# Kernel tuning notes

Measured on AMD Instinct MI355X. Metric: run time of the kernel, lower is better.

The kernel has to match this reference:

```python
import jax, jax.numpy as jnp
import numpy as np

B_, L, D_MODEL = 8, 2048, 512
EXPAND, D_STATE, HEADDIM, NGROUPS, D_CONV = 2, 16, 64, 1, 4
D_INNER = EXPAND * D_MODEL            # 1024
NHEADS = D_INNER // HEADDIM           # 16
CONV_DIM = D_INNER + 2 * NGROUPS * D_STATE   # 1056
D_IN_PROJ = 2 * D_INNER + 2 * NGROUPS * D_STATE + NHEADS  # 2096
EPS = 1e-5


def _mamba_params(key):
    ks = jax.random.split(key, 5)
    in_proj_w = jax.random.normal(ks[0], (D_IN_PROJ, D_MODEL), jnp.float32) * (D_MODEL ** -0.5)
    conv_w = jax.random.normal(ks[1], (CONV_DIM, 1, D_CONV), jnp.float32) * (D_CONV ** -0.5)
    conv_b = jnp.zeros((CONV_DIM,), jnp.float32)
    # inverse-softplus of dt ~ U[1e-3, 0.1] (mamba-ssm style init)
    dt_bias = jnp.log(jnp.expm1(jax.random.uniform(ks[2], (NHEADS,), jnp.float32, 1e-3, 0.1)))
    A_log = jnp.log(jax.random.uniform(ks[3], (NHEADS,), jnp.float32, 1.0, 16.0))
    Dp = jnp.ones((NHEADS,), jnp.float32)
    norm_w = jnp.ones((D_INNER,), jnp.float32)
    out_proj_w = jax.random.normal(ks[4], (D_MODEL, D_INNER), jnp.float32) * (D_INNER ** -0.5)
    return [in_proj_w, conv_w, conv_b, dt_bias, A_log, Dp, norm_w, out_proj_w]


def setup_inputs() -> dict:
    key = jax.random.key(0)
    k0, k1, k2 = jax.random.split(key, 3)
    d = {"x": jax.random.normal(k0, (B_, L, D_MODEL), jnp.float32)}
    names = ["in_proj_w", "conv_w", "conv_b", "dt_bias", "A_log", "Dp", "norm_w", "out_proj_w"]
    for pre, k in (("fwd_", k1), ("bwd_", k2)):
        for n, p in zip(names, _mamba_params(k)):
            d[pre + n] = p
    return d


def _silu(v):
    return v * jax.nn.sigmoid(v)


def _mamba2(u, in_proj_w, conv_w, conv_b, dt_bias, A_log, Dp, norm_w, out_proj_w):
    b, l, _ = u.shape
    zxbcdt = u @ in_proj_w.T                                # (b,l,D_IN_PROJ)
    z, xBC, dt = jnp.split(zxbcdt, [D_INNER, D_INNER + CONV_DIM], axis=-1)
    # causal depthwise conv1d + silu
    xc = jnp.transpose(xBC, (0, 2, 1))                      # (b,C,l)
    xc = jax.lax.conv_general_dilated(xc, conv_w, (1,), [(D_CONV - 1, 0)],
                                      feature_group_count=CONV_DIM)
    xBC = _silu(jnp.transpose(xc, (0, 2, 1)) + conv_b)      # (b,l,C)
    xs, Bm, Cm = jnp.split(xBC, [D_INNER, D_INNER + NGROUPS * D_STATE], axis=-1)
    xs = xs.reshape(b, l, NHEADS, HEADDIM)
    Bm = Bm.reshape(b, l, NGROUPS, D_STATE)[:, :, 0]        # ngroups=1 -> (b,l,N)
    Cm = Cm.reshape(b, l, NGROUPS, D_STATE)[:, :, 0]
    dt = jax.nn.softplus(dt + dt_bias)                      # (b,l,H)
    A = -jnp.exp(A_log)                                     # (H,)
    dA = jnp.exp(dt * A)                                    # (b,l,H), in (0,1)

    def step(h, inp):
        dA_t, dt_t, x_t, B_t, C_t = inp
        h = h * dA_t[:, :, None, None] + jnp.einsum('bh,bhp,bn->bhpn', dt_t, x_t, B_t)
        y = jnp.einsum('bhpn,bn->bhp', h, C_t)
        return h, y

    h0 = jnp.zeros((b, NHEADS, HEADDIM, D_STATE), u.dtype)
    seq = (jnp.moveaxis(dA, 1, 0), jnp.moveaxis(dt, 1, 0), jnp.moveaxis(xs, 1, 0),
           jnp.moveaxis(Bm, 1, 0), jnp.moveaxis(Cm, 1, 0))
    _, ys = jax.lax.scan(step, h0, seq)
    y = jnp.moveaxis(ys, 0, 1) + xs * Dp[None, None, :, None]   # (b,l,H,P)
    y = y.reshape(b, l, D_INNER)
    # RMSNormGated (norm_before_gate=False): rmsnorm(y * silu(z)) * w
    y = y * _silu(z)
    y = y * jax.lax.rsqrt(jnp.mean(y * y, axis=-1, keepdims=True) + EPS) * norm_w
    return y @ out_proj_w.T


def reference(x,
              fwd_in_proj_w, fwd_conv_w, fwd_conv_b, fwd_dt_bias, fwd_A_log, fwd_Dp, fwd_norm_w, fwd_out_proj_w,
              bwd_in_proj_w, bwd_conv_w, bwd_conv_b, bwd_dt_bias, bwd_A_log, bwd_Dp, bwd_norm_w, bwd_out_proj_w):
    fwd = _mamba2(x, fwd_in_proj_w, fwd_conv_w, fwd_conv_b, fwd_dt_bias, fwd_A_log, fwd_Dp, fwd_norm_w, fwd_out_proj_w)
    bwd = _mamba2(x[:, ::-1], bwd_in_proj_w, bwd_conv_w, bwd_conv_b, bwd_dt_bias, bwd_A_log, bwd_Dp, bwd_norm_w, bwd_out_proj_w)
    return fwd + bwd[:, ::-1]
```

## Files before the change

### kernel.cpp

```cpp
#include <hip/hip_runtime.h>
#include <stdint.h>

#define L_SEQ   2048
#define BATCH   8
#define DMODEL  512
#define DINNER  1024
#define NHEADS  16
#define HEADDIM 64
#define DSTATE  16
#define CONVDIM 1056
#define DINPROJ 2096
#define NPROJ   4192
#define NPROJ_P 4224
#define NROWS   (BATCH*L_SEQ)
#define NCH     32
#define CHLEN   64
#define XBCW    1072

typedef __attribute__((ext_vector_type(8))) short short8;
typedef __attribute__((ext_vector_type(4))) float f32x4;

static __device__ __forceinline__ unsigned short f2bf(float f) {
    unsigned int u = __float_as_uint(f);
    u += 0x7FFF + ((u >> 16) & 1);
    return (unsigned short)(u >> 16);
}
static __device__ __forceinline__ float bf2f(unsigned short u) {
    return __uint_as_float((unsigned int)u << 16);
}
static __device__ __forceinline__ float silu(float v) {
    return v / (1.f + __expf(-v));
}
static __device__ __forceinline__ void glds16(const unsigned short* g, unsigned short* l) {
    __builtin_amdgcn_global_load_lds(
        (const __attribute__((address_space(1))) unsigned int*)g,
        (__attribute__((address_space(3))) unsigned int*)l, 16, 0, 0);
}

#define PREP_N1 (NROWS*DMODEL)
#define PREP_N2 (NPROJ_P*DMODEL)
#define PREP_N3 (512*2048)
__global__ void k_prep(const float* __restrict__ x,
                       const float* __restrict__ fwi, const float* __restrict__ bwi,
                       const float* __restrict__ fow, const float* __restrict__ bow,
                       unsigned short* __restrict__ XB, unsigned short* __restrict__ W1,
                       unsigned short* __restrict__ W2) {
    int i = blockIdx.x * 256 + threadIdx.x;
    if (i < PREP_N1) {
        XB[i] = f2bf(x[i]);
    } else if (i < PREP_N1 + PREP_N2) {
        int j = i - PREP_N1;
        const int FS = DINPROJ * DMODEL;
        W1[j] = (j < 2 * FS) ? f2bf(j < FS ? fwi[j] : bwi[j - FS]) : 0;
    } else if (i < PREP_N1 + PREP_N2 + PREP_N3) {
        int j = i - PREP_N1 - PREP_N2;
        int n = j >> 11, k = j & 2047;
        float v = (k < DINNER) ? fow[n * DINNER + k] : bow[n * DINNER + k - DINNER];
        W2[j] = f2bf(v);
    }
}

#define BM 128
#define BN 128
#define BK 32

#define GEMM_BODY(NROUNDS, EPILOGUE)                                                        \
    __shared__ __align__(16) unsigned short as[2][BM][BK];                                  \
    __shared__ __align__(16) unsigned short bs[2][BN][BK];                                  \
    const int tid = threadIdx.x;                                                            \
    const int lane = tid & 63;                                                              \
    const int wave = tid >> 6;                                                              \
    const int wm = (wave & 1) * 64;                                                         \
    const int wn = (wave >> 1) * 64;                                                        \
    const int l16 = lane & 15;                                                              \
    const int q = lane >> 4;                                                                \
    const int sr = wave * 32;                                                               \
    const int lr = lane >> 2;                                                               \
    const int lc = (lane & 3) * 8;                                                          \
    f32x4 acc[4][4];                                                                        \
    for (int i = 0; i < 4; i++)                                                             \
        for (int j = 0; j < 4; j++) acc[i][j] = (f32x4){0.f, 0.f, 0.f, 0.f};                \
    const unsigned short* Ab = A + (size_t)(bm + sr + lr) * K + koff + lc;                  \
    const unsigned short* Bb = Bw + (size_t)(bn + sr + lr) * K + koff + lc;                 \
    glds16(Ab, &as[0][sr][0]);                                                              \
    glds16(Ab + (size_t)16 * K, &as[0][sr + 16][0]);                                        \
    glds16(Bb, &bs[0][sr][0]);                                                              \
    glds16(Bb + (size_t)16 * K, &bs[0][sr + 16][0]);                                        \
    __syncthreads();                                                                        \
    for (int r = 0; r < NROUNDS; r++) {                                                     \
        const int pb = r & 1;                                                               \
        if (r + 1 < NROUNDS) {               \
            const int kb = (r + 1) * BK;                                                    \
            glds16(Ab + kb, &as[pb ^ 1][sr][0]);                                            \
            glds16(Ab + (size_t)16 * K + kb, &as[pb ^ 1][sr + 16][0]);                      \
            glds16(Bb + kb, &bs[pb ^ 1][sr][0]);                                            \
            glds16(Bb + (size_t)16 * K + kb, &bs[pb ^ 1][sr + 16][0]);                      \
        }                                                                                   \
        short8 af[4], bfr[4];                                                               \
        for (int i = 0; i < 4; i++) af[i] = *(const short8*)&as[pb][wm + i * 16 + l16][q * 8]; \
        for (int j = 0; j < 4; j++) bfr[j] = *(const short8*)&bs[pb][wn + j * 16 + l16][q * 8]; \
        for (int i = 0; i < 4; i++)                                                         \
            for (int j = 0; j < 4; j++)                                                     \
                acc[i][j] = __builtin_amdgcn_mfma_f32_16x16x32_bf16(af[i], bfr[j], acc[i][j], 0, 0, 0); \
        __syncthreads();                          \
    }                                                                                       \
    EPILOGUE

__global__ __launch_bounds__(256, 4) void k_gemm_proj(const unsigned short* __restrict__ A,
                                                      const unsigned short* __restrict__ Bw,
                                                      unsigned short* __restrict__ ZG,
                                                      unsigned short* __restrict__ XBCDT) {
    const int K = DMODEL;
    const int N = NPROJ;
    const int lin = blockIdx.x;
    const int xcd = lin & 7;
    const int idx = lin >> 3;
    const int mloc = idx & 15;
    const int n_tile = idx >> 4;
    const int bm = (mloc * 8 + xcd) * BM;
    const int bn = n_tile * BN;
    const int koff = 0;
    GEMM_BODY(16, {
        for (int i = 0; i < 4; i++) {
            int row0 = bm + wm + i * 16 + q * 4;
            for (int j = 0; j < 4; j++) {
                int col = bn + wn + j * 16 + l16;
                if (col < N) {
                    int dir = col >= DINPROJ;
                    int cc = col - dir * DINPROJ;
                    for (int r = 0; r < 4; r++) {
                        unsigned short v = f2bf(acc[i][j][r]);
                        size_t rowo = (size_t)(dir * NROWS + row0 + r);
                        if (cc < DINNER)
                            ZG[rowo * DINNER + cc] = v;
                        else
                            XBCDT[rowo * XBCW + (cc - DINNER)] = v;
                    }
                }
            }
        }
    })
}

__global__ __launch_bounds__(256) void k_gemm_out(const unsigned short* __restrict__ A,
                                                  const unsigned short* __restrict__ Bw,
                                                  float* __restrict__ C) {
    const int K = 2048;
    const int lin = blockIdx.x;
    const int xcd = lin & 7;
    const int idx = lin >> 3;
    const int mloc = idx & 15;
    const int n_tile = idx >> 4;
    const int bm = (mloc * 8 + xcd) * BM;
    const int bn = n_tile * BN;
    const int koff = 0;
    GEMM_BODY(64, {
        for (int i = 0; i < 4; i++) {
            int row0 = bm + wm + i * 16 + q * 4;
            for (int j = 0; j < 4; j++) {
                int col = bn + wn + j * 16 + l16;
                for (int r = 0; r < 4; r++)
                    C[(size_t)(row0 + r) * 512 + col] = acc[i][j][r];
            }
        }
    })
}

__global__ __launch_bounds__(256) void k_conv2(const unsigned short* __restrict__ XBCDT,
                                               const float* __restrict__ fw_w, const float* __restrict__ fw_b,
                                               const float* __restrict__ bw_w, const float* __restrict__ bw_b,
                                               unsigned short* __restrict__ XS, float* __restrict__ BCb) {
    __shared__ unsigned short sm[70][256];
    int t = threadIdx.x;
    int bidx = blockIdx.x;
    int lcn = bidx & 31;
    int b   = (bidx >> 5) & 7;
    int dir = (bidx >> 8) & 1;
    int ct  = bidx >> 9;
    int c0 = ct * 256;
    int l0 = lcn * 64;
    int c = c0 + t;
    const unsigned short* src = XBCDT + (size_t)dir * NROWS * XBCW;
    {
        const int rr = t >> 5;
        const int ch = t & 31;
        const int cc0 = c0 + ch * 8;
        const bool cok16 = (cc0 + 8 <= XBCW);
        const short8 z8 = {0, 0, 0, 0, 0, 0, 0, 0};
#pragma unroll
        for (int pass = 0; pass < 9; ++pass) {
            int r = pass * 8 + rr;
            if (r < 70) {
                int li = l0 - 3 + r;
                short8 v = z8;
                if (li >= 0 && li < L_SEQ && cok16)
                    v = *(const short8*)&src[(size_t)((b << 11) + li) * XBCW + cc0];
                *(short8*)&sm[r][ch * 8] = v;
            }
        }
    }
    __syncthreads();
    if (c >= CONVDIM) return;
    const float* w = (dir ? bw_w : fw_w) + c * 4;
    float bias = (dir ? bw_b : fw_b)[c];
    float wr[4];
    if (dir) { wr[0] = w[3]; wr[1] = w[2]; wr[2] = w[1]; wr[3] = w[0]; }
    else     { wr[0] = w[0]; wr[1] = w[1]; wr[2] = w[2]; wr[3] = w[3]; }
    int o = dir ? 3 : 0;
    float w0 = bf2f(sm[o][t]), w1 = bf2f(sm[o + 1][t]), w2 = bf2f(sm[o + 2][t]);
    unsigned short* xso = XS + (size_t)dir * NROWS * DINNER;
    float* bco = BCb + (size_t)dir * NROWS * 32;
    int rowbase = (b << 11) + l0;
#pragma unroll 4
    for (int l = 0; l < 64; l++) {
        float w3 = bf2f(sm[l + o + 3][t]);
        float acc = ((wr[0] * w0 + wr[1] * w1) + (wr[2] * w2 + wr[3] * w3)) + bias;
        float v = silu(acc);
        int row = rowbase + l;
        if (c < DINNER)
            xso[(size_t)row * DINNER + c] = f2bf(v);
        else
            bco[(size_t)row * 32 + (c - DINNER)] = v;
        w0 = w1; w1 = w2; w2 = w3;
    }
}

__global__ void k_dt(const unsigned short* __restrict__ XBCDT,
                     const float* __restrict__ fdtb, const float* __restrict__ fAl,
                     const float* __restrict__ bdtb, const float* __restrict__ bAl,
                     float* __restrict__ DT, float* __restrict__ DA) {
    int gid = blockIdx.x * 256 + threadIdx.x;
    if (gid >= 2 * NROWS * NHEADS) return;
    int h = gid & 15;
    int row = (gid >> 4) & (NROWS - 1);
    int dir = gid >> 18;
    float dtb = (dir ? bdtb : fdtb)[h];
    float Al = (dir ? bAl : fAl)[h];
    float x = bf2f(XBCDT[(size_t)(dir * NROWS + row) * XBCW + CONVDIM + h]) + dtb;
    float dt = (x > 15.f) ? x : log1pf(__expf(x));
    float dA = __expf(-__expf(Al) * dt);
    DT[gid] = dt;
    DA[gid] = dA;
}

__global__ __launch_bounds__(64) void k_scan_state(const unsigned short* __restrict__ XS,
                                                   const float* __restrict__ BCb,
                                                   const float* __restrict__ DT,
                                                   const float* __restrict__ DA,
                                                   float* __restrict__ S, float* __restrict__ P) {
    int idx = blockIdx.x;
    int c = idx & 31, hp = (idx >> 5) & 7, b = (idx >> 8) & 7, dir = idx >> 11;
    int t = threadIdx.x;
    int h = hp * 2 + (t >> 5);
    int p0 = (t & 31) * 2;
    const unsigned short* xs = XS + (size_t)dir * NROWS * DINNER;
    const float* bc = BCb + (size_t)dir * NROWS * 32;
    const float* dtp = DT + (size_t)dir * NROWS * NHEADS;
    const float* dap = DA + (size_t)dir * NROWS * NHEADS;
    float hreg0[16], hreg1[16];
#pragma unroll
    for (int n = 0; n < 16; n++) { hreg0[n] = 0.f; hreg1[n] = 0.f; }
    float Pp = 1.f;
#pragma unroll 2
    for (int tl = 0; tl < CHLEN; ++tl) {
        int tt = c * CHLEN + tl;
        int l = dir ? (L_SEQ - 1 - tt) : tt;
        int row = (b << 11) + l;
        unsigned int xv2 = *(const unsigned int*)&xs[(size_t)row * DINNER + h * HEADDIM + p0];
        float xv0 = bf2f((unsigned short)(xv2 & 0xffff));
        float xv1 = bf2f((unsigned short)(xv2 >> 16));
        float dt = dtp[row * 16 + h];
        float dA = dap[row * 16 + h];
        f32x4 Bv[4];
#pragma unroll
        for (int qq = 0; qq < 4; qq++) Bv[qq] = *(const f32x4*)&bc[(size_t)row * 32 + qq * 4];
        float k0 = dt * xv0, k1 = dt * xv1;
#pragma unroll
        for (int n = 0; n < 16; n++) {
            float bv = Bv[n >> 2][n & 3];
            hreg0[n] = fmaf(hreg0[n], dA, k0 * bv);
            hreg1[n] = fmaf(hreg1[n], dA, k1 * bv);
        }
        Pp *= dA;
    }
    int sh = (((dir * 8 + b) * 16 + h) * NCH + c);
#pragma unroll
    for (int qq = 0; qq < 4; qq++) {
        f32x4 v0 = {hreg0[qq * 4], hreg0[qq * 4 + 1], hreg0[qq * 4 + 2], hreg0[qq * 4 + 3]};
        f32x4 v1 = {hreg1[qq * 4], hreg1[qq * 4 + 1], hreg1[qq * 4 + 2], hreg1[qq * 4 + 3]};
        *(f32x4*)&S[(size_t)sh * 1024 + p0 * 16 + qq * 4] = v0;
        *(f32x4*)&S[(size_t)sh * 1024 + (p0 + 1) * 16 + qq * 4] = v1;
    }
    if ((t & 31) == 0) P[sh] = Pp;
}

__global__ void k_combine(float* __restrict__ S, const float* __restrict__ P) {
    int gid = blockIdx.x * 256 + threadIdx.x;
    if (gid >= 2 * 8 * 16 * 1024) return;
    int pn = gid & 1023;
    int base = gid >> 10;
    float H = 0.f;
#pragma unroll 4
    for (int c = 0; c < NCH; c++) {
        size_t o = ((size_t)base * NCH + c) * 1024 + pn;
        float s = S[o];
        S[o] = H;
        H = H * P[base * NCH + c] + s;
    }
}

__global__ __launch_bounds__(64) void k_scan_out(const unsigned short* __restrict__ XS,
                                                 const float* __restrict__ BCb,
                                                 const float* __restrict__ DT,
                                                 const float* __restrict__ DA,
                                                 const float* __restrict__ Hinit,
                                                 const float* __restrict__ fDp,
                                                 const float* __restrict__ bDp,
                                                 unsigned short* __restrict__ Y) {
    int idx = blockIdx.x;
    int c = idx & 31, hp = (idx >> 5) & 7, b = (idx >> 8) & 7, dir = idx >> 11;
    int t = threadIdx.x;
    int h = hp * 2 + (t >> 5);
    int p0 = (t & 31) * 2;
    const unsigned short* xs = XS + (size_t)dir * NROWS * DINNER;
    const float* bc = BCb + (size_t)dir * NROWS * 32;
    const float* dtp = DT + (size_t)dir * NROWS * NHEADS;
    const float* dap = DA + (size_t)dir * NROWS * NHEADS;
    unsigned short* yo = Y + (size_t)dir * NROWS * DINNER;
    float Dpv = (dir ? bDp : fDp)[h];
    int sh = (((dir * 8 + b) * 16 + h) * NCH + c);
    float hreg0[16], hreg1[16];
#pragma unroll
    for (int qq = 0; qq < 4; qq++) {
        f32x4 v0 = *(const f32x4*)&Hinit[(size_t)sh * 1024 + p0 * 16 + qq * 4];
        f32x4 v1 = *(const f32x4*)&Hinit[(size_t)sh * 1024 + (p0 + 1) * 16 + qq * 4];
#pragma unroll
        for (int e = 0; e < 4; e++) { hreg0[qq * 4 + e] = v0[e]; hreg1[qq * 4 + e] = v1[e]; }
    }
#pragma unroll 2
    for (int tl = 0; tl < CHLEN; ++tl) {
        int tt = c * CHLEN + tl;
        int l = dir ? (L_SEQ - 1 - tt) : tt;
        int row = (b << 11) + l;
        unsigned int xv2 = *(const unsigned int*)&xs[(size_t)row * DINNER + h * HEADDIM + p0];
        float xv0 = bf2f((unsigned short)(xv2 & 0xffff));
        float xv1 = bf2f((unsigned short)(xv2 >> 16));
        float dt = dtp[row * 16 + h];
        float dA = dap[row * 16 + h];
        f32x4 Bv[4], Cv[4];
#pragma unroll
        for (int qq = 0; qq < 4; qq++) Bv[qq] = *(const f32x4*)&bc[(size_t)row * 32 + qq * 4];
#pragma unroll
        for (int qq = 0; qq < 4; qq++) Cv[qq] = *(const f32x4*)&bc[(size_t)row * 32 + 16 + qq * 4];
        float k0 = dt * xv0, k1 = dt * xv1;
        float y0 = 0.f, y1 = 0.f;
#pragma unroll
        for (int n = 0; n < 16; n++) {
            float bv = Bv[n >> 2][n & 3];
            float cv = Cv[n >> 2][n & 3];
            hreg0[n] = fmaf(hreg0[n], dA, k0 * bv);
            hreg1[n] = fmaf(hreg1[n], dA, k1 * bv);
            y0 = fmaf(hreg0[n], cv, y0);
            y1 = fmaf(hreg1[n], cv, y1);
        }
        unsigned int yw = (unsigned int)f2bf(y0 + xv0 * Dpv)
                        | ((unsigned int)f2bf(y1 + xv1 * Dpv) << 16);
        *(unsigned int*)&yo[(size_t)row * DINNER + h * HEADDIM + p0] = yw;
    }
}

__global__ __launch_bounds__(256) void k_gatenorm(const unsigned short* __restrict__ Y,
                                                  const unsigned short* __restrict__ ZG,
                                                  const float* __restrict__ fnw,
                                                  const float* __restrict__ bnw,
                                                  unsigned short* __restrict__ NRM) {
    int bid = blockIdx.x;
    int t = threadIdx.x;
    int sub = t >> 7;
    int tt = t & 127;
    int rid = bid * 2 + sub;
    int dir = rid >> 14;
    int row = rid & (NROWS - 1);
    int c = tt * 8;
    const size_t base = (size_t)(dir * NROWS + row) * DINNER + c;
    uint4 yu = *(const uint4*)&Y[base];
    uint4 zu = *(const uint4*)&ZG[base];
    float v[8];
    {
        const unsigned int yw[4] = {yu.x, yu.y, yu.z, yu.w};
        const unsigned int zw[4] = {zu.x, zu.y, zu.z, zu.w};
#pragma unroll
        for (int e = 0; e < 4; e++) {
            v[e * 2]     = bf2f((unsigned short)(yw[e] & 0xffff)) * silu(bf2f((unsigned short)(zw[e] & 0xffff)));
            v[e * 2 + 1] = bf2f((unsigned short)(yw[e] >> 16))    * silu(bf2f((unsigned short)(zw[e] >> 16)));
        }
    }
    float ss = 0.f;
#pragma unroll
    for (int e = 0; e < 8; e++) ss += v[e] * v[e];
#pragma unroll
    for (int off = 32; off > 0; off >>= 1) ss += __shfl_down(ss, off);
    __shared__ float red[4];
    if ((t & 63) == 0) red[t >> 6] = ss;
    __syncthreads();
    float tot = red[sub * 2] + red[sub * 2 + 1];
    float scale = rsqrtf(tot * (1.f / 1024.f) + 1e-5f);
    const float* nw = (dir ? bnw : fnw) + c;
    f32x4 nw0 = *(const f32x4*)&nw[0];
    f32x4 nw1 = *(const f32x4*)&nw[4];
    unsigned int ow[4];
#pragma unroll
    for (int e = 0; e < 4; e++) {
        float a = v[e * 2]     * scale * (e < 2 ? nw0[e * 2]     : nw1[(e - 2) * 2]);
        float b = v[e * 2 + 1] * scale * (e < 2 ? nw0[e * 2 + 1] : nw1[(e - 2) * 2 + 1]);
        ow[e] = (unsigned int)f2bf(a) | ((unsigned int)f2bf(b) << 16);
    }
    uint4 o = {ow[0], ow[1], ow[2], ow[3]};
    *(uint4*)&NRM[(size_t)row * 2048 + dir * DINNER + c] = o;
}

extern "C" void kernel_launch(void* const* d_in, const int* in_sizes, int n_in,
                              void* d_out, int out_size, void* d_ws, size_t ws_size,
                              hipStream_t stream) {
    const float* x     = (const float*)d_in[0];
    const float* f_inw = (const float*)d_in[1];
    const float* f_cw  = (const float*)d_in[2];
    const float* f_cb  = (const float*)d_in[3];
    const float* f_dtb = (const float*)d_in[4];
    const float* f_Al  = (const float*)d_in[5];
    const float* f_Dp  = (const float*)d_in[6];
    const float* f_nw  = (const float*)d_in[7];
    const float* f_ow  = (const float*)d_in[8];
    const float* b_inw = (const float*)d_in[9];
    const float* b_cw  = (const float*)d_in[10];
    const float* b_cb  = (const float*)d_in[11];
    const float* b_dtb = (const float*)d_in[12];
    const float* b_Al  = (const float*)d_in[13];
    const float* b_Dp  = (const float*)d_in[14];
    const float* b_nw  = (const float*)d_in[15];
    const float* b_ow  = (const float*)d_in[16];

    char* ws = (char*)d_ws;
    size_t off = 0;
    auto alloc = [&](size_t bytes) {
        void* p = ws + off;
        off += (bytes + 255) & ~(size_t)255;
        return p;
    };
    unsigned short* XBCDT = (unsigned short*)alloc((size_t)2 * NROWS * XBCW * 2);
    unsigned short* NRM   = XBCDT;
    float* S = (float*)XBCDT;
    float* P = (float*)((char*)XBCDT + (size_t)2 * 8 * 16 * NCH * 1024 * 4);
    unsigned short* XS    = (unsigned short*)alloc((size_t)2 * NROWS * DINNER * 2);
    unsigned short* Yb    = XS;
    unsigned short* ZG    = (unsigned short*)alloc((size_t)2 * NROWS * DINNER * 2);
    unsigned short* W2    = (unsigned short*)alloc((size_t)512 * 2048 * 2);
    float* BCb  = (float*)alloc((size_t)2 * NROWS * 32 * 4);
    float* DT   = (float*)alloc((size_t)2 * NROWS * NHEADS * 4);
    float* DA   = (float*)alloc((size_t)2 * NROWS * NHEADS * 4);
    char* unionBase = (char*)alloc((size_t)16777216 + (size_t)NPROJ_P * DMODEL * 2);
    unsigned short* XB = (unsigned short*)unionBase;
    unsigned short* W1 = (unsigned short*)(unionBase + 16777216);

    if (ws_size < off) return;

    {
        int n = PREP_N1 + PREP_N2 + PREP_N3;
        k_prep<<<(n + 255) / 256, 256, 0, stream>>>(x, f_inw, b_inw, f_ow, b_ow, XB, W1, W2);
    }
    k_gemm_proj<<<8 * 16 * 33, 256, 0, stream>>>(XB, W1, ZG, XBCDT);
    k_conv2<<<5 * 2 * 8 * 32, 256, 0, stream>>>(XBCDT, f_cw, f_cb, b_cw, b_cb, XS, BCb);
    {
        int n = 2 * NROWS * NHEADS;
        k_dt<<<(n + 255) / 256, 256, 0, stream>>>(XBCDT, f_dtb, f_Al, b_dtb, b_Al, DT, DA);
    }
    k_scan_state<<<2 * 8 * 8 * NCH, 64, 0, stream>>>(XS, BCb, DT, DA, S, P);
    {
        int n = 2 * 8 * 16 * 1024;
        k_combine<<<(n + 255) / 256, 256, 0, stream>>>(S, P);
    }
    k_scan_out<<<2 * 8 * 8 * NCH, 64, 0, stream>>>(XS, BCb, DT, DA, S, f_Dp, b_Dp, Yb);
    k_gatenorm<<<NROWS, 256, 0, stream>>>(Yb, ZG, f_nw, b_nw, NRM);
    k_gemm_out<<<8 * 16 * 4, 256, 0, stream>>>(NRM, W2, (float*)d_out);
}
```

Baseline: 469.0 us.

## Fuse gating and sum-of-squares into scan output, vectorize prep, shrink out-GEMM tile

The silu(z) gate and per-row sum of squares move into the scan output kernel, which accumulates them with atomics into a new SSQ buffer that the combine kernel zeroes. The gatenorm kernel then only rescales and no longer reads Z or does a block reduction. The prep conversion kernel now handles four elements per thread with vector loads. The output GEMM uses 64-row tiles so it launches twice as many blocks, and the scan loops are unrolled by 4. The cost is many float atomics per row and per-row sums computed from unrounded values where the old path used bf16-rounded ones.

New measurement: 479.5 us (median of 2 runs). +2.3%, slower.

```diff
diff --git a/kernel.cpp b/kernel.cpp
--- a/kernel.cpp
+++ b/kernel.cpp
@@ -40,23 +40,35 @@
 #define PREP_N1 (NROWS*DMODEL)
 #define PREP_N2 (NPROJ_P*DMODEL)
 #define PREP_N3 (512*2048)
+#define PREP_T  ((PREP_N1+PREP_N2+PREP_N3)/4)
+static __device__ __forceinline__ uint2 pack4(float4 v) {
+    uint2 o;
+    o.x = (unsigned int)f2bf(v.x) | ((unsigned int)f2bf(v.y) << 16);
+    o.y = (unsigned int)f2bf(v.z) | ((unsigned int)f2bf(v.w) << 16);
+    return o;
+}
 __global__ void k_prep(const float* __restrict__ x,
                        const float* __restrict__ fwi, const float* __restrict__ bwi,
                        const float* __restrict__ fow, const float* __restrict__ bow,
                        unsigned short* __restrict__ XB, unsigned short* __restrict__ W1,
                        unsigned short* __restrict__ W2) {
     int i = blockIdx.x * 256 + threadIdx.x;
-    if (i < PREP_N1) {
-        XB[i] = f2bf(x[i]);
-    } else if (i < PREP_N1 + PREP_N2) {
-        int j = i - PREP_N1;
+    if (i >= PREP_T) return;
+    int j4 = i * 4;
+    if (j4 < PREP_N1) {
+        *(uint2*)&XB[j4] = pack4(*(const float4*)&x[j4]);
+    } else if (j4 < PREP_N1 + PREP_N2) {
+        int j = j4 - PREP_N1;
         const int FS = DINPROJ * DMODEL;
-        W1[j] = (j < 2 * FS) ? f2bf(j < FS ? fwi[j] : bwi[j - FS]) : 0;
-    } else if (i < PREP_N1 + PREP_N2 + PREP_N3) {
-        int j = i - PREP_N1 - PREP_N2;
+        uint2 o = {0u, 0u};
+        if (j < 2 * FS)
+            o = pack4(j < FS ? *(const float4*)&fwi[j] : *(const float4*)&bwi[j - FS]);
+        *(uint2*)&W1[j] = o;
+    } else {
+        int j = j4 - PREP_N1 - PREP_N2;
         int n = j >> 11, k = j & 2047;
-        float v = (k < DINNER) ? fow[n * DINNER + k] : bow[n * DINNER + k - DINNER];
-        W2[j] = f2bf(v);
+        const float* s = (k < DINNER) ? &fow[n * DINNER + k] : &bow[n * DINNER + k - DINNER];
+        *(uint2*)&W2[j] = pack4(*(const float4*)s);
     }
 }
 
@@ -106,6 +118,47 @@
     }                                                                                       \
     EPILOGUE
 
+#define GEMM_BODY_OUT(NROUNDS, EPILOGUE)                                                    \
+    __shared__ __align__(16) unsigned short as[2][64][BK];                                  \
+    __shared__ __align__(16) unsigned short bs[2][BN][BK];                                  \
+    const int tid = threadIdx.x;                                                            \
+    const int lane = tid & 63;                                                              \
+    const int wave = tid >> 6;                                                              \
+    const int wm = (wave & 1) * 32;                                                         \
+    const int wn = (wave >> 1) * 64;                                                        \
+    const int l16 = lane & 15;                                                              \
+    const int q = lane >> 4;                                                                \
+    const int sra = wave * 16;                                                              \
+    const int srb = wave * 32;                                                              \
+    const int lr = lane >> 2;                                                               \
+    const int lc = (lane & 3) * 8;                                                          \
+    f32x4 acc[2][4];                                                                        \
+    for (int i = 0; i < 2; i++)                                                             \
+        for (int j = 0; j < 4; j++) acc[i][j] = (f32x4){0.f, 0.f, 0.f, 0.f};                \
+    const unsigned short* Ab = A + (size_t)(bm + sra + lr) * K + koff + lc;                 \
+    const unsigned short* Bb = Bw + (size_t)(bn + srb + lr) * K + koff + lc;                \
+    glds16(Ab, &as[0][sra][0]);                                                             \
+    glds16(Bb, &bs[0][srb][0]);                                                             \
+    glds16(Bb + (size_t)16 * K, &bs[0][srb + 16][0]);                                       \
+    __syncthreads();                                                                        \
+    for (int r = 0; r < NROUNDS; r++) {                                                     \
+        const int pb = r & 1;                                                               \
+        if (r + 1 < NROUNDS) {                                                              \
+            const int kb = (r + 1) * BK;                                                    \
+            glds16(Ab + kb, &as[pb ^ 1][sra][0]);                                           \
+            glds16(Bb + kb, &bs[pb ^ 1][srb][0]);                                           \
+            glds16(Bb + (size_t)16 * K + kb, &bs[pb ^ 1][srb + 16][0]);                     \
+        }                                                                                   \
+        short8 af[2], bfr[4];                                                               \
+        for (int i = 0; i < 2; i++) af[i] = *(const short8*)&as[pb][wm + i * 16 + l16][q * 8]; \
+        for (int j = 0; j < 4; j++) bfr[j] = *(const short8*)&bs[pb][wn + j * 16 + l16][q * 8]; \
+        for (int i = 0; i < 2; i++)                                                         \
+            for (int j = 0; j < 4; j++)                                                     \
+                acc[i][j] = __builtin_amdgcn_mfma_f32_16x16x32_bf16(af[i], bfr[j], acc[i][j], 0, 0, 0); \
+        __syncthreads();                                                                    \
+    }                                                                                       \
+    EPILOGUE
+
 __global__ __launch_bounds__(256, 4) void k_gemm_proj(const unsigned short* __restrict__ A,
                                                       const unsigned short* __restrict__ Bw,
                                                       unsigned short* __restrict__ ZG,
@@ -149,13 +202,13 @@
     const int lin = blockIdx.x;
     const int xcd = lin & 7;
     const int idx = lin >> 3;
-    const int mloc = idx & 15;
-    const int n_tile = idx >> 4;
-    const int bm = (mloc * 8 + xcd) * BM;
+    const int mloc = idx & 31;
+    const int n_tile = idx >> 5;
+    const int bm = (mloc * 8 + xcd) * 64;
     const int bn = n_tile * BN;
     const int koff = 0;
-    GEMM_BODY(64, {
-        for (int i = 0; i < 4; i++) {
+    GEMM_BODY_OUT(64, {
+        for (int i = 0; i < 2; i++) {
             int row0 = bm + wm + i * 16 + q * 4;
             for (int j = 0; j < 4; j++) {
                 int col = bn + wn + j * 16 + l16;
@@ -261,7 +314,7 @@
 #pragma unroll
     for (int n = 0; n < 16; n++) { hreg0[n] = 0.f; hreg1[n] = 0.f; }
     float Pp = 1.f;
-#pragma unroll 2
+#pragma unroll 4
     for (int tl = 0; tl < CHLEN; ++tl) {
         int tt = c * CHLEN + tl;
         int l = dir ? (L_SEQ - 1 - tt) : tt;
@@ -294,8 +347,10 @@
     if ((t & 31) == 0) P[sh] = Pp;
 }
 
-__global__ void k_combine(float* __restrict__ S, const float* __restrict__ P) {
+__global__ void k_combine(float* __restrict__ S, const float* __restrict__ P,
+                          float* __restrict__ SSQ) {
     int gid = blockIdx.x * 256 + threadIdx.x;
+    if (gid < 2 * NROWS) SSQ[gid] = 0.f;
     if (gid >= 2 * 8 * 16 * 1024) return;
     int pn = gid & 1023;
     int base = gid >> 10;
@@ -316,6 +371,8 @@
                                                  const float* __restrict__ Hinit,
                                                  const float* __restrict__ fDp,
                                                  const float* __restrict__ bDp,
+                                                 const unsigned short* __restrict__ ZG,
+                                                 float* __restrict__ SSQ,
                                                  unsigned short* __restrict__ Y) {
     int idx = blockIdx.x;
     int c = idx & 31, hp = (idx >> 5) & 7, b = (idx >> 8) & 7, dir = idx >> 11;
@@ -323,10 +380,12 @@
     int h = hp * 2 + (t >> 5);
     int p0 = (t & 31) * 2;
     const unsigned short* xs = XS + (size_t)dir * NROWS * DINNER;
+    const unsigned short* zgd = ZG + (size_t)dir * NROWS * DINNER;
     const float* bc = BCb + (size_t)dir * NROWS * 32;
     const float* dtp = DT + (size_t)dir * NROWS * NHEADS;
     const float* dap = DA + (size_t)dir * NROWS * NHEADS;
     unsigned short* yo = Y + (size_t)dir * NROWS * DINNER;
+    float* ssqd = SSQ + (size_t)dir * NROWS;
     float Dpv = (dir ? bDp : fDp)[h];
     int sh = (((dir * 8 + b) * 16 + h) * NCH + c);
     float hreg0[16], hreg1[16];
@@ -337,7 +396,7 @@
 #pragma unroll
         for (int e = 0; e < 4; e++) { hreg0[qq * 4 + e] = v0[e]; hreg1[qq * 4 + e] = v1[e]; }
     }
-#pragma unroll 2
+#pragma unroll 4
     for (int tl = 0; tl < CHLEN; ++tl) {
         int tt = c * CHLEN + tl;
         int l = dir ? (L_SEQ - 1 - tt) : tt;
@@ -363,14 +422,20 @@
             y0 = fmaf(hreg0[n], cv, y0);
             y1 = fmaf(hreg1[n], cv, y1);
         }
-        unsigned int yw = (unsigned int)f2bf(y0 + xv0 * Dpv)
-                        | ((unsigned int)f2bf(y1 + xv1 * Dpv) << 16);
+        unsigned int zz = *(const unsigned int*)&zgd[(size_t)row * DINNER + h * HEADDIM + p0];
+        float v0 = (y0 + xv0 * Dpv) * silu(bf2f((unsigned short)(zz & 0xffff)));
+        float v1 = (y1 + xv1 * Dpv) * silu(bf2f((unsigned short)(zz >> 16)));
+        unsigned int yw = (unsigned int)f2bf(v0) | ((unsigned int)f2bf(v1) << 16);
         *(unsigned int*)&yo[(size_t)row * DINNER + h * HEADDIM + p0] = yw;
+        float pr = v0 * v0 + v1 * v1;
+#pragma unroll
+        for (int off = 16; off > 0; off >>= 1) pr += __shfl_down(pr, off);
+        if ((t & 31) == 0) atomicAdd(&ssqd[row], pr);
     }
 }
 
 __global__ __launch_bounds__(256) void k_gatenorm(const unsigned short* __restrict__ Y,
-                                                  const unsigned short* __restrict__ ZG,
+                                                  const float* __restrict__ SSQ,
                                                   const float* __restrict__ fnw,
                                                   const float* __restrict__ bnw,
                                                   unsigned short* __restrict__ NRM) {
@@ -382,37 +447,20 @@
     int dir = rid >> 14;
     int row = rid & (NROWS - 1);
     int c = tt * 8;
-    const size_t base = (size_t)(dir * NROWS + row) * DINNER + c;
+    const size_t base = (size_t)rid * DINNER + c;
     uint4 yu = *(const uint4*)&Y[base];
-    uint4 zu = *(const uint4*)&ZG[base];
-    float v[8];
-    {
-        const unsigned int yw[4] = {yu.x, yu.y, yu.z, yu.w};
-        const unsigned int zw[4] = {zu.x, zu.y, zu.z, zu.w};
-#pragma unroll
-        for (int e = 0; e < 4; e++) {
-            v[e * 2]     = bf2f((unsigned short)(yw[e] & 0xffff)) * silu(bf2f((unsigned short)(zw[e] & 0xffff)));
-            v[e * 2 + 1] = bf2f((unsigned short)(yw[e] >> 16))    * silu(bf2f((unsigned short)(zw[e] >> 16)));
-        }
-    }
-    float ss = 0.f;
-#pragma unroll
-    for (int e = 0; e < 8; e++) ss += v[e] * v[e];
-#pragma unroll
-    for (int off = 32; off > 0; off >>= 1) ss += __shfl_down(ss, off);
-    __shared__ float red[4];
-    if ((t & 63) == 0) red[t >> 6] = ss;
-    __syncthreads();
-    float tot = red[sub * 2] + red[sub * 2 + 1];
-    float scale = rsqrtf(tot * (1.f / 1024.f) + 1e-5f);
+    float scale = rsqrtf(SSQ[rid] * (1.f / 1024.f) + 1e-5f);
     const float* nw = (dir ? bnw : fnw) + c;
     f32x4 nw0 = *(const f32x4*)&nw[0];
     f32x4 nw1 = *(const f32x4*)&nw[4];
+    const unsigned int yw[4] = {yu.x, yu.y, yu.z, yu.w};
     unsigned int ow[4];
 #pragma unroll
     for (int e = 0; e < 4; e++) {
-        float a = v[e * 2]     * scale * (e < 2 ? nw0[e * 2]     : nw1[(e - 2) * 2]);
-        float b = v[e * 2 + 1] * scale * (e < 2 ? nw0[e * 2 + 1] : nw1[(e - 2) * 2 + 1]);
+        float a = bf2f((unsigned short)(yw[e] & 0xffff)) * scale
+                * (e < 2 ? nw0[e * 2]     : nw1[(e - 2) * 2]);
+        float b = bf2f((unsigned short)(yw[e] >> 16)) * scale
+                * (e < 2 ? nw0[e * 2 + 1] : nw1[(e - 2) * 2 + 1]);
         ow[e] = (unsigned int)f2bf(a) | ((unsigned int)f2bf(b) << 16);
     }
     uint4 o = {ow[0], ow[1], ow[2], ow[3]};
@@ -458,16 +506,14 @@
     float* BCb  = (float*)alloc((size_t)2 * NROWS * 32 * 4);
     float* DT   = (float*)alloc((size_t)2 * NROWS * NHEADS * 4);
     float* DA   = (float*)alloc((size_t)2 * NROWS * NHEADS * 4);
+    float* SSQ  = (float*)alloc((size_t)2 * NROWS * 4);
     char* unionBase = (char*)alloc((size_t)16777216 + (size_t)NPROJ_P * DMODEL * 2);
     unsigned short* XB = (unsigned short*)unionBase;
     unsigned short* W1 = (unsigned short*)(unionBase + 16777216);
 
     if (ws_size < off) return;
 
-    {
-        int n = PREP_N1 + PREP_N2 + PREP_N3;
-        k_prep<<<(n + 255) / 256, 256, 0, stream>>>(x, f_inw, b_inw, f_ow, b_ow, XB, W1, W2);
-    }
+    k_prep<<<(PREP_T + 255) / 256, 256, 0, stream>>>(x, f_inw, b_inw, f_ow, b_ow, XB, W1, W2);
     k_gemm_proj<<<8 * 16 * 33, 256, 0, stream>>>(XB, W1, ZG, XBCDT);
     k_conv2<<<5 * 2 * 8 * 32, 256, 0, stream>>>(XBCDT, f_cw, f_cb, b_cw, b_cb, XS, BCb);
     {
@@ -477,9 +523,9 @@
     k_scan_state<<<2 * 8 * 8 * NCH, 64, 0, stream>>>(XS, BCb, DT, DA, S, P);
     {
         int n = 2 * 8 * 16 * 1024;
-        k_combine<<<(n + 255) / 256, 256, 0, stream>>>(S, P);
-    }
-    k_scan_out<<<2 * 8 * 8 * NCH, 64, 0, stream>>>(XS, BCb, DT, DA, S, f_Dp, b_Dp, Yb);
-    k_gatenorm<<<NROWS, 256, 0, stream>>>(Yb, ZG, f_nw, b_nw, NRM);
-    k_gemm_out<<<8 * 16 * 4, 256, 0, stream>>>(NRM, W2, (float*)d_out);
-}
+        k_combine<<<(n + 255) / 256, 256, 0, stream>>>(S, P, SSQ);
+    }
+    k_scan_out<<<2 * 8 * 8 * NCH, 64, 0, stream>>>(XS, BCb, DT, DA, S, f_Dp, b_Dp, ZG, SSQ, Yb);
+    k_gatenorm<<<NROWS, 256, 0, stream>>>(Yb, SSQ, f_nw, b_nw, NRM);
+    k_gemm_out<<<8 * 32 * 4, 256, 0, stream>>>(NRM, W2, (float*)d_out);
+}
```

## Vectorize prep conversion, raise scan unroll, add occupancy hint to output GEMM

Applied to the files above, without the earlier changes.

The fp32-to-bf16 prep kernel now handles four elements per thread, using float4 loads and packed 8-byte stores, so it issues fewer and wider memory operations. The chunk-scan loops are unrolled by 4 instead of 2 to expose more independent loads per iteration. The output GEMM gets a minimum of 4 blocks per SM in its launch bounds, which may cap registers and cause spills.

Result: faster. 459.2 us, median of 2 (-2.1%).

```diff
diff --git a/kernel.cpp b/kernel.cpp
--- a/kernel.cpp
+++ b/kernel.cpp
@@ -40,23 +40,35 @@
 #define PREP_N1 (NROWS*DMODEL)
 #define PREP_N2 (NPROJ_P*DMODEL)
 #define PREP_N3 (512*2048)
+#define PREP_T  ((PREP_N1+PREP_N2+PREP_N3)/4)
+static __device__ __forceinline__ uint2 pack4(float4 v) {
+    uint2 o;
+    o.x = (unsigned int)f2bf(v.x) | ((unsigned int)f2bf(v.y) << 16);
+    o.y = (unsigned int)f2bf(v.z) | ((unsigned int)f2bf(v.w) << 16);
+    return o;
+}
 __global__ void k_prep(const float* __restrict__ x,
                        const float* __restrict__ fwi, const float* __restrict__ bwi,
                        const float* __restrict__ fow, const float* __restrict__ bow,
                        unsigned short* __restrict__ XB, unsigned short* __restrict__ W1,
                        unsigned short* __restrict__ W2) {
     int i = blockIdx.x * 256 + threadIdx.x;
-    if (i < PREP_N1) {
-        XB[i] = f2bf(x[i]);
-    } else if (i < PREP_N1 + PREP_N2) {
-        int j = i - PREP_N1;
+    if (i >= PREP_T) return;
+    int j4 = i * 4;
+    if (j4 < PREP_N1) {
+        *(uint2*)&XB[j4] = pack4(*(const float4*)&x[j4]);
+    } else if (j4 < PREP_N1 + PREP_N2) {
+        int j = j4 - PREP_N1;
         const int FS = DINPROJ * DMODEL;
-        W1[j] = (j < 2 * FS) ? f2bf(j < FS ? fwi[j] : bwi[j - FS]) : 0;
-    } else if (i < PREP_N1 + PREP_N2 + PREP_N3) {
-        int j = i - PREP_N1 - PREP_N2;
+        uint2 o = {0u, 0u};
+        if (j < 2 * FS)
+            o = pack4(j < FS ? *(const float4*)&fwi[j] : *(const float4*)&bwi[j - FS]);
+        *(uint2*)&W1[j] = o;
+    } else {
+        int j = j4 - PREP_N1 - PREP_N2;
         int n = j >> 11, k = j & 2047;
-        float v = (k < DINNER) ? fow[n * DINNER + k] : bow[n * DINNER + k - DINNER];
-        W2[j] = f2bf(v);
+        const float* s = (k < DINNER) ? &fow[n * DINNER + k] : &bow[n * DINNER + k - DINNER];
+        *(uint2*)&W2[j] = pack4(*(const float4*)s);
     }
 }
 
@@ -142,9 +154,9 @@
     })
 }
 
-__global__ __launch_bounds__(256) void k_gemm_out(const unsigned short* __restrict__ A,
-                                                  const unsigned short* __restrict__ Bw,
-                                                  float* __restrict__ C) {
+__global__ __launch_bounds__(256, 4) void k_gemm_out(const unsigned short* __restrict__ A,
+                                                     const unsigned short* __restrict__ Bw,
+                                                     float* __restrict__ C) {
     const int K = 2048;
     const int lin = blockIdx.x;
     const int xcd = lin & 7;
@@ -261,7 +273,7 @@
 #pragma unroll
     for (int n = 0; n < 16; n++) { hreg0[n] = 0.f; hreg1[n] = 0.f; }
     float Pp = 1.f;
-#pragma unroll 2
+#pragma unroll 4
     for (int tl = 0; tl < CHLEN; ++tl) {
         int tt = c * CHLEN + tl;
         int l = dir ? (L_SEQ - 1 - tt) : tt;
@@ -337,7 +349,7 @@
 #pragma unroll
         for (int e = 0; e < 4; e++) { hreg0[qq * 4 + e] = v0[e]; hreg1[qq * 4 + e] = v1[e]; }
     }
-#pragma unroll 2
+#pragma unroll 4
     for (int tl = 0; tl < CHLEN; ++tl) {
         int tt = c * CHLEN + tl;
         int l = dir ? (L_SEQ - 1 - tt) : tt;
@@ -464,10 +476,7 @@
 
     if (ws_size < off) return;
 
-    {
-        int n = PREP_N1 + PREP_N2 + PREP_N3;
-        k_prep<<<(n + 255) / 256, 256, 0, stream>>>(x, f_inw, b_inw, f_ow, b_ow, XB, W1, W2);
-    }
+    k_prep<<<(PREP_T + 255) / 256, 256, 0, stream>>>(x, f_inw, b_inw, f_ow, b_ow, XB, W1, W2);
     k_gemm_proj<<<8 * 16 * 33, 256, 0, stream>>>(XB, W1, ZG, XBCDT);
     k_conv2<<<5 * 2 * 8 * 32, 256, 0, stream>>>(XBCDT, f_cw, f_cb, b_cw, b_cb, XS, BCb);
     {
```
